# Kernel tuning notes

Hardware: AMD Instinct MI355X
Metric: run time of the kernel (lower is better)

Reference implementation:

```python
import jax, jax.numpy as jnp
import numpy as np

G, N, E = 64, 1000, 8192          # graphs, nodes/graph, edges/graph
F_IN, C, H, HID, NCLS = 128, 128, 4, 256, 2
EPS = 1e-5


def _gcn(x, src, dst, W, b):
    # GCNConv: symmetric normalization with self-loops, sum aggregation.
    h = x @ W                                              # [N, C]
    deg = jax.ops.segment_sum(jnp.ones(E, h.dtype), dst, num_segments=N) + 1.0
    dinv = jax.lax.rsqrt(deg)                              # deg^{-1/2}
    msg = h[src] * (dinv[src] * dinv[dst])[:, None]        # [E, C] gather
    out = jax.ops.segment_sum(msg, dst, num_segments=N)    # scatter-add
    out = out + h * (dinv * dinv)[:, None]                 # self-loop term
    return out + b


def _layernorm(y, g, b):
    mu = y.mean(-1, keepdims=True)
    var = ((y - mu) ** 2).mean(-1, keepdims=True)
    return (y - mu) * jax.lax.rsqrt(var + EPS) * g + b


def setup_inputs() -> dict:
    key = jax.random.key(0)
    ks = jax.random.split(key, 12)
    rn = lambda k, s: jax.random.normal(k, s, jnp.float32) * 0.05
    return dict(
        x=jax.random.normal(ks[0], (G, N, F_IN), jnp.float32),
        edge_index=jax.random.randint(ks[1], (G, 2, E), 0, N),
        W0=rn(ks[2], (F_IN, C)), b0=jnp.zeros((C,), jnp.float32),
        W1=rn(ks[3], (C, C)), b1=jnp.zeros((C,), jnp.float32),
        in_w=rn(ks[4], (3 * C, C)), in_b=jnp.zeros((3 * C,), jnp.float32),
        out_w=rn(ks[5], (C, C)), out_b=jnp.zeros((C,), jnp.float32),
        ln2_g=jnp.ones((C,), jnp.float32), ln2_b=jnp.zeros((C,), jnp.float32),
        mw1=rn(ks[6], (C, HID)), mb1=jnp.zeros((HID,), jnp.float32),
        mw2=rn(ks[7], (HID, C)), mb2=jnp.zeros((C,), jnp.float32),
        lw=rn(ks[8], (C, NCLS)), lb=jnp.zeros((NCLS,), jnp.float32),
    )


def reference(x, edge_index, W0, b0, W1, b1, in_w, in_b, out_w, out_b,
              ln2_g, ln2_b, mw1, mb1, mw2, mb2, lw, lb):
    src, dst = edge_index[:, 0, :], edge_index[:, 1, :]
    conv = jax.vmap(_gcn, in_axes=(0, 0, 0, None, None))
    h = jnp.tanh(conv(x, src, dst, W0, b0))   # [G, N, C]
    h = jnp.tanh(conv(h, src, dst, W1, b1))
    g = h.sum(axis=1)                          # SumAggregation -> [G, C]

    # MultiheadAttention, unbatched: sequence of G graph embeddings
    qkv = g @ in_w.T + in_b
    q, k, v = jnp.split(qkv, 3, axis=-1)
    d = C // H
    qh, kh, vh = (t.reshape(G, H, d) for t in (q, k, v))
    attn = jax.nn.softmax(jnp.einsum('qhd,khd->hqk', qh, kh) * (d ** -0.5), axis=-1)
    o = jnp.einsum('hqk,khd->qhd', attn, vh).reshape(G, C) @ out_w.T + out_b

    x_attend = o                               # dropout = identity (eval)
    # NOTE: original computes layer_norm1(x_attend) but immediately overwrites it.
    mlp = jnp.maximum(x_attend @ mw1 + mb1, 0.0) @ mw2 + mb2
    y = _layernorm(x_attend + mlp, ln2_g, ln2_b)
    node_repr = jnp.maximum(y, 0.0).sum(axis=0)  # [C]
    return node_repr @ lw + lb                   # [NCLS]
```

## Files before the change

kernel.cpp:

```cpp
#include <hip/hip_runtime.h>
#include <math.h>

#define Gn 64
#define Nn 1000
#define En 8192
#define Cc 128
#define HIDn 256
#define EPSf 1e-5f

typedef __attribute__((ext_vector_type(8))) short bh8;
typedef __attribute__((ext_vector_type(4))) float fx4;

__device__ __forceinline__ unsigned short f2bf(float f) {
    unsigned u = __float_as_uint(f);
    u += 0x7fffu + ((u >> 16) & 1u);
    return (unsigned short)(u >> 16);
}
__device__ __forceinline__ float bflo(unsigned u) { return __uint_as_float(u << 16); }
__device__ __forceinline__ float bfhi(unsigned u) { return __uint_as_float(u & 0xffff0000u); }
__device__ __forceinline__ float tanh_fast(float x) {
    float e = exp2f(x * 2.885390081777927f);
    return 1.f - 2.f * __builtin_amdgcn_rcpf(e + 1.f);
}

__global__ __launch_bounds__(256) void k_wt(const float* __restrict__ W0, const float* __restrict__ W1,
                                            unsigned short* __restrict__ Wt0g,
                                            unsigned short* __restrict__ Wt1g)
{
    __shared__ __align__(16) short Wls[128][136];
    int t = threadIdx.x;
    const float* Wsrc = (blockIdx.x == 0) ? W0 : W1;
    unsigned short* Wdst = (blockIdx.x == 0) ? Wt0g : Wt1g;
    for (int idx = t; idx < 16384; idx += 256) {
        int kI = idx >> 7, n = idx & 127;
        Wls[n][kI] = (short)f2bf(Wsrc[idx]);
    }
    __syncthreads();
    for (int idx = t; idx < 2048; idx += 256) {
        int n = idx >> 4, kc = idx & 15;
        *(bh8*)(Wdst + (size_t)idx * 8) = *(const bh8*)&Wls[n][kc * 8];
    }
}

__global__ __launch_bounds__(512) void k_front(const int* __restrict__ ei, const float* __restrict__ X,
                                               const unsigned short* __restrict__ Wt0g,
                                               int4* __restrict__ ninfo, int2* __restrict__ epair,
                                               float* __restrict__ pooled, float* __restrict__ repr,
                                               int* __restrict__ bars,
                                               unsigned short* __restrict__ Hout)
{
    __shared__ __align__(16) short Wt[128][136];
    __shared__ int wsum[8];
    int t = threadIdx.x;
    int b = blockIdx.x;

    if (b < 64) {
        int* curs = (int*)&Wt[0][0];
        float* dinv_s = (float*)((char*)&Wt[0][0] + 4096);
        int g = b;
        const int* srcp = ei + (size_t)g * 2 * En;
        const int* dstp = srcp + En;
        int lane = t & 63, wv = t >> 6;

        curs[t * 2] = 0; curs[t * 2 + 1] = 0;
        __syncthreads();
        for (int e = t; e < En; e += 512) atomicAdd(&curs[dstp[e]], 1);
        __syncthreads();

        int base = t * 2;
        int d0 = curs[base], d1 = curs[base + 1];
        int s = d0 + d1;
        int v = s;
        #pragma unroll
        for (int off = 1; off <= 32; off <<= 1) {
            int u = __shfl_up(v, off);
            if (lane >= off) v += u;
        }
        if (lane == 63) wsum[wv] = v;
        __syncthreads();
        int woff = 0;
        #pragma unroll
        for (int w = 0; w < 8; ++w) if (w < wv) woff += wsum[w];
        int e0 = woff + v - s;
        int e1 = e0 + d0;
        float dv0 = rsqrtf((float)d0 + 1.f), dv1 = rsqrtf((float)d1 + 1.f);
        curs[base] = e0; curs[base + 1] = e1;
        dinv_s[base] = dv0; dinv_s[base + 1] = dv1;
        if (base < Nn)     ninfo[g * Nn + base]     = make_int4(e0, d0, __float_as_int(dv0 * dv0), 0);
        if (base + 1 < Nn) ninfo[g * Nn + base + 1] = make_int4(e1, d1, __float_as_int(dv1 * dv1), 0);
        __syncthreads();

        for (int e = t; e < En; e += 512) {
            int dd = dstp[e], ss = srcp[e];
            int p = atomicAdd(&curs[dd], 1);
            float w = dinv_s[ss] * dinv_s[dd];
            epair[(size_t)g * En + p] = make_int2(ss << 8, __float_as_int(w));
        }
        if (t < Cc) pooled[g * Cc + t] = 0.f;
        if (g == 0 && t < Cc) repr[t] = 0.f;
        if (g == 0 && t < 4) bars[t] = 0;
        return;
    }

    int bb = b - 64;
    int xcd = bb & 7, gg = (bb >> 3) & 7, rblk = bb >> 6;
    int g = xcd + 8 * gg;
    for (int idx = t; idx < 2048; idx += 512) {
        int n = idx >> 4, kc = idx & 15;
        *(bh8*)&Wt[n][kc * 8] = *(const bh8*)(Wt0g + (size_t)idx * 8);
    }
    __syncthreads();

    int wave = t >> 6, l = t & 63;
    int lr = l & 15, lg = l >> 4;
    const float* Xf = X + (size_t)g * Nn * Cc;
    unsigned short* Hg = Hout + (size_t)g * Nn * Cc;

    int rbase = rblk * 128 + wave * 16;
    int r = rbase + lr;
    bool ok = r < Nn;
    bh8 af[4];
    #pragma unroll
    for (int ks = 0; ks < 4; ++ks) {
        if (ok) {
            const float* xp = Xf + (size_t)r * Cc + ks * 32 + lg * 8;
            fx4 a0 = *(const fx4*)xp;
            fx4 a1 = *(const fx4*)(xp + 4);
            bh8 av;
            av[0] = (short)f2bf(a0[0]); av[1] = (short)f2bf(a0[1]);
            av[2] = (short)f2bf(a0[2]); av[3] = (short)f2bf(a0[3]);
            av[4] = (short)f2bf(a1[0]); av[5] = (short)f2bf(a1[1]);
            av[6] = (short)f2bf(a1[2]); av[7] = (short)f2bf(a1[3]);
            af[ks] = av;
        } else af[ks] = bh8{0, 0, 0, 0, 0, 0, 0, 0};
    }
    fx4 acc[8];
    #pragma unroll
    for (int ct = 0; ct < 8; ++ct) acc[ct] = fx4{0.f, 0.f, 0.f, 0.f};
    #pragma unroll
    for (int ks = 0; ks < 4; ++ks) {
        #pragma unroll
        for (int ct = 0; ct < 8; ++ct) {
            bh8 bfr = *(const bh8*)(&Wt[ct * 16 + lr][ks * 32 + lg * 8]);
            acc[ct] = __builtin_amdgcn_mfma_f32_16x16x32_bf16(af[ks], bfr, acc[ct], 0, 0, 0);
        }
    }
    #pragma unroll
    for (int ct = 0; ct < 8; ++ct) {
        #pragma unroll
        for (int rg = 0; rg < 4; ++rg) {
            int row = rbase + lg * 4 + rg;
            if (row < Nn) Hg[(size_t)row * Cc + ct * 16 + lr] = f2bf(acc[ct][rg]);
        }
    }
}

__global__ __launch_bounds__(256) void k_gemm1(const unsigned short* __restrict__ Xh,
                                               const unsigned short* __restrict__ Wtg,
                                               unsigned short* __restrict__ Hout)
{
    __shared__ __align__(16) short Wt[128][136];
    int b = blockIdx.x;
    int xcd = b & 7, gg = (b >> 3) & 7, rblk = b >> 6;
    int g = xcd + 8 * gg;
    int t = threadIdx.x;
    for (int idx = t; idx < 2048; idx += 256) {
        int n = idx >> 4, kc = idx & 15;
        bh8 v = *(const bh8*)(Wtg + (size_t)idx * 8);
        *(bh8*)&Wt[n][kc * 8] = v;
    }
    __syncthreads();

    int wave = t >> 6, l = t & 63;
    int lr = l & 15, lg = l >> 4;
    const short* Xg = (const short*)Xh + (size_t)g * Nn * Cc;
    unsigned short* Hg = Hout + (size_t)g * Nn * Cc;

    int rbase = rblk * 64 + wave * 16;
    int r = rbase + lr;
    bool ok = r < Nn;
    bh8 af[4];
    #pragma unroll
    for (int ks = 0; ks < 4; ++ks) {
        if (ok) af[ks] = *(const bh8*)(Xg + (size_t)r * Cc + ks * 32 + lg * 8);
        else    af[ks] = bh8{0, 0, 0, 0, 0, 0, 0, 0};
    }
    fx4 acc[8];
    #pragma unroll
    for (int ct = 0; ct < 8; ++ct) acc[ct] = fx4{0.f, 0.f, 0.f, 0.f};
    #pragma unroll
    for (int ks = 0; ks < 4; ++ks) {
        #pragma unroll
        for (int ct = 0; ct < 8; ++ct) {
            bh8 bfr = *(const bh8*)(&Wt[ct * 16 + lr][ks * 32 + lg * 8]);
            acc[ct] = __builtin_amdgcn_mfma_f32_16x16x32_bf16(af[ks], bfr, acc[ct], 0, 0, 0);
        }
    }
    #pragma unroll
    for (int ct = 0; ct < 8; ++ct) {
        #pragma unroll
        for (int rg = 0; rg < 4; ++rg) {
            int row = rbase + lg * 4 + rg;
            if (row < Nn) Hg[(size_t)row * Cc + ct * 16 + lr] = f2bf(acc[ct][rg]);
        }
    }
}

template<int POOL>
__global__ __launch_bounds__(256) void k_combine(const unsigned* __restrict__ Hb, const int2* __restrict__ epair,
                                                 const int4* __restrict__ ninfo, const float* __restrict__ bias,
                                                 unsigned* __restrict__ Tout, float* __restrict__ pooled)
{
    int b = blockIdx.x;
    int xcd = b & 7, j = b >> 3;
    int g = xcd + 8 * (j & 7);
    int blk = j >> 3;
    int wave = threadIdx.x >> 6, lane = threadIdx.x & 63;
    const char* Hgc = (const char*)(Hb + (size_t)g * Nn * 64);
    const int2* epg = epair + (size_t)g * En;
    const int4* nig = ninfo + (size_t)g * Nn;
    float2 bb = *(const float2*)(bias + lane * 2);
    int lb4 = lane * 4;
    float px = 0.f, py = 0.f;
    for (int n = blk * 4 + wave; n < Nn; n += 128) {
        int4 ni = nig[n];
        int st = ni.x, dc = ni.y;
        float sw = __int_as_float(ni.z);
        unsigned hv = *(const unsigned*)(Hgc + n * 256 + lb4);
        float a0x = bflo(hv) * sw + bb.x, a0y = bfhi(hv) * sw + bb.y;
        float a1x = 0.f, a1y = 0.f, a2x = 0.f, a2y = 0.f, a3x = 0.f, a3y = 0.f;
        int e = 0;
        for (; e + 4 <= dc; e += 4) {
            int2 p0 = epg[st + e];
            int2 p1 = epg[st + e + 1];
            int2 p2 = epg[st + e + 2];
            int2 p3 = epg[st + e + 3];
            unsigned r0 = *(const unsigned*)(Hgc + p0.x + lb4);
            unsigned r1 = *(const unsigned*)(Hgc + p1.x + lb4);
            unsigned r2 = *(const unsigned*)(Hgc + p2.x + lb4);
            unsigned r3 = *(const unsigned*)(Hgc + p3.x + lb4);
            float w0 = __int_as_float(p0.y), w1 = __int_as_float(p1.y);
            float w2 = __int_as_float(p2.y), w3 = __int_as_float(p3.y);
            a0x = fmaf(bflo(r0), w0, a0x); a0y = fmaf(bfhi(r0), w0, a0y);
            a1x = fmaf(bflo(r1), w1, a1x); a1y = fmaf(bfhi(r1), w1, a1y);
            a2x = fmaf(bflo(r2), w2, a2x); a2y = fmaf(bfhi(r2), w2, a2y);
            a3x = fmaf(bflo(r3), w3, a3x); a3y = fmaf(bfhi(r3), w3, a3y);
        }
        for (; e < dc; ++e) {
            int2 p0 = epg[st + e];
            unsigned r0 = *(const unsigned*)(Hgc + p0.x + lb4);
            float w0 = __int_as_float(p0.y);
            a0x = fmaf(bflo(r0), w0, a0x); a0y = fmaf(bfhi(r0), w0, a0y);
        }
        float ax = (a0x + a1x) + (a2x + a3x);
        float ay = (a0y + a1y) + (a2y + a3y);
        float tx = tanh_fast(ax), ty = tanh_fast(ay);
        if (POOL) { px += tx; py += ty; }
        else Tout[(size_t)(g * Nn + n) * 64 + lane] = ((unsigned)f2bf(ty) << 16) | (unsigned)f2bf(tx);
    }
    if (POOL) {
        atomicAdd(&pooled[g * Cc + lane * 2], px);
        atomicAdd(&pooled[g * Cc + lane * 2 + 1], py);
    }
}

__global__ __launch_bounds__(1024) void k_qkv(const float* __restrict__ pooled, const float* __restrict__ in_w,
                                              const float* __restrict__ in_b, float* __restrict__ qkvb)
{
    int t = threadIdx.x, lane = t & 63, wv = t >> 6;
    int c = blockIdx.x * 16 + wv;
    const float* wr = in_w + c * Cc;
    float w0 = wr[lane], w1 = wr[64 + lane];
    float bias = in_b[c];
    for (int i = 0; i < Gn; ++i) {
        float p = fmaf(pooled[i * Cc + lane], w0, pooled[i * Cc + 64 + lane] * w1);
        #pragma unroll
        for (int off2 = 32; off2 > 0; off2 >>= 1) p += __shfl_xor(p, off2);
        if (lane == 0) qkvb[i * 384 + c] = p + bias;
    }
}

__global__ __launch_bounds__(512) void k_tail(const float* __restrict__ qkvb, const float* __restrict__ out_w,
                                              const float* __restrict__ out_b, const float* __restrict__ mw1,
                                              const float* __restrict__ mb1, const float* __restrict__ mw2,
                                              const float* __restrict__ mb2, const float* __restrict__ ln2g,
                                              const float* __restrict__ ln2b, const float* __restrict__ lw,
                                              const float* __restrict__ lb, float* __restrict__ repr,
                                              int* __restrict__ ctr, float* __restrict__ out)
{
    __shared__ float kk[64][129];
    __shared__ float vv[64][129];
    __shared__ float qrow[128];
    __shared__ float S[4][64];
    __shared__ float sob[128];
    __shared__ float sxatt[128];
    __shared__ float sm1p[2][256];
    __shared__ float sm1[256];
    __shared__ float sp2[4][128];
    __shared__ float yb[128];
    __shared__ int slast;
    int g = blockIdx.x;
    int t = threadIdx.x, lane = t & 63, wv = t >> 6;

    for (int idx = t; idx < 8192; idx += 512) {
        int i = idx >> 7, c = idx & 127;
        kk[i][c] = qkvb[i * 384 + 128 + c];
        vv[i][c] = qkvb[i * 384 + 256 + c];
    }
    if (t < 128) qrow[t] = qkvb[g * 384 + t];
    __syncthreads();

    if (t < 256) {
        int h = t >> 6, jj = t & 63;
        int base = h * 32;
        float acc = 0.f;
        #pragma unroll
        for (int d = 0; d < 32; ++d) acc = fmaf(qrow[base + d], kk[jj][base + d], acc);
        S[h][jj] = acc * 0.17677669529663687f;
    }
    __syncthreads();
    if (wv < 4) {
        float val = S[wv][lane];
        float m = val;
        #pragma unroll
        for (int off = 32; off > 0; off >>= 1) m = fmaxf(m, __shfl_xor(m, off));
        float e2 = expf(val - m);
        float ssum = e2;
        #pragma unroll
        for (int off = 32; off > 0; off >>= 1) ssum += __shfl_xor(ssum, off);
        S[wv][lane] = e2 / ssum;
    }
    __syncthreads();
    if (t < 128) {
        int h = t >> 5, d = t & 31;
        int col = h * 32 + d;
        float acc = 0.f;
        #pragma unroll 4
        for (int j = 0; j < 64; ++j) acc = fmaf(S[h][j], vv[j][col], acc);
        sob[col] = acc;
    }
    __syncthreads();

    {
        float o0 = sob[lane], o1 = sob[64 + lane];
        for (int c = wv; c < Cc; c += 8) {
            const float* wr = out_w + c * Cc;
            float p = fmaf(o0, wr[lane], o1 * wr[64 + lane]);
            #pragma unroll
            for (int off = 32; off > 0; off >>= 1) p += __shfl_xor(p, off);
            if (lane == 0) sxatt[c] = p + out_b[c];
        }
    }
    __syncthreads();

    {
        int jc = t & 255, half = t >> 8;
        int k0b = half * 64;
        float a[8];
        #pragma unroll
        for (int u = 0; u < 8; ++u) a[u] = 0.f;
        for (int k0 = k0b; k0 < k0b + 64; k0 += 8) {
            #pragma unroll
            for (int u = 0; u < 8; ++u)
                a[u] = fmaf(sxatt[k0 + u], mw1[(size_t)(k0 + u) * HIDn + jc], a[u]);
        }
        sm1p[half][jc] = ((a[0] + a[1]) + (a[2] + a[3])) + ((a[4] + a[5]) + (a[6] + a[7]));
        __syncthreads();
        if (t < 256) sm1[t] = fmaxf(sm1p[0][t] + sm1p[1][t] + mb1[t], 0.f);
    }
    __syncthreads();

    {
        int c = t & 127, q = t >> 7;
        int j0b = q * 64;
        float a[8];
        #pragma unroll
        for (int u = 0; u < 8; ++u) a[u] = 0.f;
        for (int j0 = j0b; j0 < j0b + 64; j0 += 8) {
            #pragma unroll
            for (int u = 0; u < 8; ++u)
                a[u] = fmaf(sm1[j0 + u], mw2[(size_t)(j0 + u) * Cc + c], a[u]);
        }
        sp2[q][c] = ((a[0] + a[1]) + (a[2] + a[3])) + ((a[4] + a[5]) + (a[6] + a[7]));
        __syncthreads();
        if (t < 128) yb[t] = sxatt[t] + (sp2[0][t] + sp2[1][t]) + (sp2[2][t] + sp2[3][t]) + mb2[t];
    }
    __syncthreads();

    if (t < 64) {
        float v0 = yb[lane], v1 = yb[64 + lane];
        float s = v0 + v1;
        #pragma unroll
        for (int off = 32; off > 0; off >>= 1) s += __shfl_xor(s, off);
        float mu = s * (1.f / 128.f);
        float d0 = v0 - mu, d1 = v1 - mu;
        float vvr = d0 * d0 + d1 * d1;
        #pragma unroll
        for (int off = 32; off > 0; off >>= 1) vvr += __shfl_xor(vvr, off);
        float rstd = rsqrtf(vvr * (1.f / 128.f) + EPSf);
        float z0 = fmaxf(d0 * rstd * ln2g[lane] + ln2b[lane], 0.f);
        float z1 = fmaxf(d1 * rstd * ln2g[64 + lane] + ln2b[64 + lane], 0.f);
        atomicAdd(&repr[lane], z0);
        atomicAdd(&repr[64 + lane], z1);
    }

    __threadfence();
    __syncthreads();
    if (t == 0) slast = atomicAdd(ctr, 1);
    __syncthreads();
    if (slast == 63) {
        __threadfence();
        __shared__ float r0s[128], r1s[128];
        if (t < 128) {
            float r = __hip_atomic_load(&repr[t], __ATOMIC_RELAXED, __HIP_MEMORY_SCOPE_AGENT);
            r0s[t] = r * lw[t * 2 + 0];
            r1s[t] = r * lw[t * 2 + 1];
        }
        __syncthreads();
        for (int s2 = 64; s2 > 0; s2 >>= 1) {
            if (t < s2) { r0s[t] += r0s[t + s2]; r1s[t] += r1s[t + s2]; }
            __syncthreads();
        }
        if (t == 0) { out[0] = r0s[0] + lb[0]; out[1] = r1s[0] + lb[1]; }
    }
}

extern "C" void kernel_launch(void* const* d_in, const int* in_sizes, int n_in,
                              void* d_out, int out_size, void* d_ws, size_t ws_size,
                              hipStream_t stream)
{
    const float* x     = (const float*)d_in[0];
    const int*   ei    = (const int*)d_in[1];
    const float* W0    = (const float*)d_in[2];
    const float* b0    = (const float*)d_in[3];
    const float* W1    = (const float*)d_in[4];
    const float* b1    = (const float*)d_in[5];
    const float* in_w  = (const float*)d_in[6];
    const float* in_b  = (const float*)d_in[7];
    const float* out_w = (const float*)d_in[8];
    const float* out_b = (const float*)d_in[9];
    const float* ln2g  = (const float*)d_in[10];
    const float* ln2b  = (const float*)d_in[11];
    const float* mw1   = (const float*)d_in[12];
    const float* mb1   = (const float*)d_in[13];
    const float* mw2   = (const float*)d_in[14];
    const float* mb2   = (const float*)d_in[15];
    const float* lw    = (const float*)d_in[16];
    const float* lb    = (const float*)d_in[17];
    float* out = (float*)d_out;
    (void)in_sizes; (void)n_in; (void)out_size; (void)ws_size;

    char* ws = (char*)d_ws;
    size_t off = 0;
    auto carve = [&](size_t bytes) { size_t o = off; off += (bytes + 255) & ~(size_t)255; return o; };
    size_t o_ni    = carve((size_t)Gn * Nn * 16);
    size_t o_ep    = carve((size_t)Gn * En * 8);
    size_t o_pool  = carve((size_t)Gn * Cc * 4);
    size_t o_qkv   = carve((size_t)Gn * 384 * 4);
    size_t o_repr  = carve((size_t)Cc * 4);
    size_t o_bars  = carve(256);
    size_t o_W0t   = carve((size_t)Cc * Cc * 2);
    size_t o_W1t   = carve((size_t)Cc * Cc * 2);
    size_t o_H     = carve((size_t)Gn * Nn * Cc * 2);
    size_t o_T     = carve((size_t)Gn * Nn * Cc * 2);

    int4*  ninfo  = (int4*)(ws + o_ni);
    int2*  epair  = (int2*)(ws + o_ep);
    float* pooled = (float*)(ws + o_pool);
    float* qkvb   = (float*)(ws + o_qkv);
    float* repr   = (float*)(ws + o_repr);
    int*   bars   = (int*)(ws + o_bars);
    unsigned short* Wt0g = (unsigned short*)(ws + o_W0t);
    unsigned short* Wt1g = (unsigned short*)(ws + o_W1t);
    unsigned short* H  = (unsigned short*)(ws + o_H);
    unsigned short* T  = (unsigned short*)(ws + o_T);

    k_wt<<<2, 256, 0, stream>>>(W0, W1, Wt0g, Wt1g);
    k_front<<<576, 512, 0, stream>>>(ei, x, Wt0g, ninfo, epair, pooled, repr, bars, H);
    k_combine<0><<<2048, 256, 0, stream>>>((const unsigned*)H, epair, ninfo, b0, (unsigned*)T, nullptr);
    k_gemm1<<<1024, 256, 0, stream>>>(T, Wt1g, H);
    k_combine<1><<<2048, 256, 0, stream>>>((const unsigned*)H, epair, ninfo, b1, nullptr, pooled);
    k_qkv<<<24, 1024, 0, stream>>>(pooled, in_w, in_b, qkvb);
    k_tail<<<64, 512, 0, stream>>>(qkvb, out_w, out_b, mw1, mb1, mw2, mb2, ln2g, ln2b,
                                   lw, lb, repr, &bars[2], out);
}
```

Before: 152.0 us.

## Fuse first-layer aggregation with second GEMM via shared-memory tile

Merges the layer-0 edge aggregation and tanh with the layer-1 GEMM into one kernel. Each block aggregates 64 node rows into an LDS bf16 tile, then runs MFMA against the W1 tile and writes H2 directly. This drops the global write and re-read of the intermediate T buffer and one kernel launch. In exchange each block does the irregular gather work serially per wave (8 rows per wave) before the GEMM, so the gather phase has less parallelism and latency hiding than the separate 2048-block combine kernel had.

```diff
diff --git a/kernel.cpp b/kernel.cpp
--- a/kernel.cpp
+++ b/kernel.cpp
@@ -155,61 +155,109 @@
     }
 }
 
-__global__ __launch_bounds__(256) void k_gemm1(const unsigned short* __restrict__ Xh,
-                                               const unsigned short* __restrict__ Wtg,
-                                               unsigned short* __restrict__ Hout)
+__global__ __launch_bounds__(512) void k_cg1(const unsigned* __restrict__ Hb, const int2* __restrict__ epair,
+                                             const int4* __restrict__ ninfo, const float* __restrict__ bias,
+                                             const unsigned short* __restrict__ Wtg,
+                                             unsigned short* __restrict__ Hout)
 {
     __shared__ __align__(16) short Wt[128][136];
+    __shared__ __align__(16) short Tl[64][136];
     int b = blockIdx.x;
     int xcd = b & 7, gg = (b >> 3) & 7, rblk = b >> 6;
     int g = xcd + 8 * gg;
-    int t = threadIdx.x;
-    for (int idx = t; idx < 2048; idx += 256) {
+    int t = threadIdx.x, wv = t >> 6, lane = t & 63;
+
+    for (int idx = t; idx < 2048; idx += 512) {
         int n = idx >> 4, kc = idx & 15;
-        bh8 v = *(const bh8*)(Wtg + (size_t)idx * 8);
-        *(bh8*)&Wt[n][kc * 8] = v;
-    }
-    __syncthreads();
-
-    int wave = t >> 6, l = t & 63;
-    int lr = l & 15, lg = l >> 4;
-    const short* Xg = (const short*)Xh + (size_t)g * Nn * Cc;
-    unsigned short* Hg = Hout + (size_t)g * Nn * Cc;
-
-    int rbase = rblk * 64 + wave * 16;
-    int r = rbase + lr;
-    bool ok = r < Nn;
-    bh8 af[4];
-    #pragma unroll
-    for (int ks = 0; ks < 4; ++ks) {
-        if (ok) af[ks] = *(const bh8*)(Xg + (size_t)r * Cc + ks * 32 + lg * 8);
-        else    af[ks] = bh8{0, 0, 0, 0, 0, 0, 0, 0};
-    }
-    fx4 acc[8];
-    #pragma unroll
-    for (int ct = 0; ct < 8; ++ct) acc[ct] = fx4{0.f, 0.f, 0.f, 0.f};
-    #pragma unroll
-    for (int ks = 0; ks < 4; ++ks) {
-        #pragma unroll
-        for (int ct = 0; ct < 8; ++ct) {
-            bh8 bfr = *(const bh8*)(&Wt[ct * 16 + lr][ks * 32 + lg * 8]);
-            acc[ct] = __builtin_amdgcn_mfma_f32_16x16x32_bf16(af[ks], bfr, acc[ct], 0, 0, 0);
-        }
-    }
-    #pragma unroll
-    for (int ct = 0; ct < 8; ++ct) {
-        #pragma unroll
-        for (int rg = 0; rg < 4; ++rg) {
-            int row = rbase + lg * 4 + rg;
-            if (row < Nn) Hg[(size_t)row * Cc + ct * 16 + lr] = f2bf(acc[ct][rg]);
-        }
-    }
-}
-
-template<int POOL>
-__global__ __launch_bounds__(256) void k_combine(const unsigned* __restrict__ Hb, const int2* __restrict__ epair,
-                                                 const int4* __restrict__ ninfo, const float* __restrict__ bias,
-                                                 unsigned* __restrict__ Tout, float* __restrict__ pooled)
+        *(bh8*)&Wt[n][kc * 8] = *(const bh8*)(Wtg + (size_t)idx * 8);
+    }
+    __syncthreads();
+
+    {
+        const char* Hgc = (const char*)(Hb + (size_t)g * Nn * 64);
+        const int2* epg = epair + (size_t)g * En;
+        const int4* nig = ninfo + (size_t)g * Nn;
+        float2 bb = *(const float2*)(bias + lane * 2);
+        int lb4 = lane * 4;
+        int rbase = rblk * 64;
+        for (int i = 0; i < 8; ++i) {
+            int lrow = wv * 8 + i;
+            int n = rbase + lrow;
+            unsigned packed = 0;
+            if (n < Nn) {
+                int4 ni = nig[n];
+                int st = ni.x, dc = ni.y;
+                float sw = __int_as_float(ni.z);
+                unsigned hv = *(const unsigned*)(Hgc + n * 256 + lb4);
+                float a0x = bflo(hv) * sw + bb.x, a0y = bfhi(hv) * sw + bb.y;
+                float a1x = 0.f, a1y = 0.f, a2x = 0.f, a2y = 0.f, a3x = 0.f, a3y = 0.f;
+                int e = 0;
+                for (; e + 4 <= dc; e += 4) {
+                    int2 p0 = epg[st + e];
+                    int2 p1 = epg[st + e + 1];
+                    int2 p2 = epg[st + e + 2];
+                    int2 p3 = epg[st + e + 3];
+                    unsigned r0 = *(const unsigned*)(Hgc + p0.x + lb4);
+                    unsigned r1 = *(const unsigned*)(Hgc + p1.x + lb4);
+                    unsigned r2 = *(const unsigned*)(Hgc + p2.x + lb4);
+                    unsigned r3 = *(const unsigned*)(Hgc + p3.x + lb4);
+                    float w0 = __int_as_float(p0.y), w1 = __int_as_float(p1.y);
+                    float w2 = __int_as_float(p2.y), w3 = __int_as_float(p3.y);
+                    a0x = fmaf(bflo(r0), w0, a0x); a0y = fmaf(bfhi(r0), w0, a0y);
+                    a1x = fmaf(bflo(r1), w1, a1x); a1y = fmaf(bfhi(r1), w1, a1y);
+                    a2x = fmaf(bflo(r2), w2, a2x); a2y = fmaf(bfhi(r2), w2, a2y);
+                    a3x = fmaf(bflo(r3), w3, a3x); a3y = fmaf(bfhi(r3), w3, a3y);
+                }
+                for (; e < dc; ++e) {
+                    int2 p0 = epg[st + e];
+                    unsigned r0 = *(const unsigned*)(Hgc + p0.x + lb4);
+                    float w0 = __int_as_float(p0.y);
+                    a0x = fmaf(bflo(r0), w0, a0x); a0y = fmaf(bfhi(r0), w0, a0y);
+                }
+                float ax = (a0x + a1x) + (a2x + a3x);
+                float ay = (a0y + a1y) + (a2y + a3y);
+                packed = ((unsigned)f2bf(tanh_fast(ay)) << 16) | (unsigned)f2bf(tanh_fast(ax));
+            }
+            *(unsigned*)&Tl[lrow][lane * 2] = packed;
+        }
+    }
+    __syncthreads();
+
+    {
+        int lr = lane & 15, lg = lane >> 4;
+        int tb = (wv & 3) * 16;
+        int ctb = (wv >> 2) * 4;
+        unsigned short* Hg = Hout + (size_t)g * Nn * Cc;
+        int rbase = rblk * 64;
+
+        bh8 af[4];
+        #pragma unroll
+        for (int ks = 0; ks < 4; ++ks) af[ks] = *(const bh8*)&Tl[tb + lr][ks * 32 + lg * 8];
+        fx4 acc[4];
+        #pragma unroll
+        for (int c2 = 0; c2 < 4; ++c2) acc[c2] = fx4{0.f, 0.f, 0.f, 0.f};
+        #pragma unroll
+        for (int ks = 0; ks < 4; ++ks) {
+            #pragma unroll
+            for (int c2 = 0; c2 < 4; ++c2) {
+                bh8 bfr = *(const bh8*)(&Wt[(ctb + c2) * 16 + lr][ks * 32 + lg * 8]);
+                acc[c2] = __builtin_amdgcn_mfma_f32_16x16x32_bf16(af[ks], bfr, acc[c2], 0, 0, 0);
+            }
+        }
+        #pragma unroll
+        for (int c2 = 0; c2 < 4; ++c2) {
+            #pragma unroll
+            for (int rg = 0; rg < 4; ++rg) {
+                int row = rbase + tb + lg * 4 + rg;
+                if (row < Nn) Hg[(size_t)row * Cc + (ctb + c2) * 16 + lr] = f2bf(acc[c2][rg]);
+            }
+        }
+    }
+}
+
+__global__ __launch_bounds__(256) void k_combine1(const unsigned* __restrict__ Hb, const int2* __restrict__ epair,
+                                                  const int4* __restrict__ ninfo, const float* __restrict__ bias,
+                                                  float* __restrict__ pooled)
 {
     int b = blockIdx.x;
     int xcd = b & 7, j = b >> 3;
@@ -254,14 +302,11 @@
         }
         float ax = (a0x + a1x) + (a2x + a3x);
         float ay = (a0y + a1y) + (a2y + a3y);
-        float tx = tanh_fast(ax), ty = tanh_fast(ay);
-        if (POOL) { px += tx; py += ty; }
-        else Tout[(size_t)(g * Nn + n) * 64 + lane] = ((unsigned)f2bf(ty) << 16) | (unsigned)f2bf(tx);
-    }
-    if (POOL) {
-        atomicAdd(&pooled[g * Cc + lane * 2], px);
-        atomicAdd(&pooled[g * Cc + lane * 2 + 1], py);
-    }
+        px += tanh_fast(ax);
+        py += tanh_fast(ay);
+    }
+    atomicAdd(&pooled[g * Cc + lane * 2], px);
+    atomicAdd(&pooled[g * Cc + lane * 2 + 1], py);
 }
 
 __global__ __launch_bounds__(1024) void k_qkv(const float* __restrict__ pooled, const float* __restrict__ in_w,
@@ -462,7 +507,7 @@
     size_t o_W0t   = carve((size_t)Cc * Cc * 2);
     size_t o_W1t   = carve((size_t)Cc * Cc * 2);
     size_t o_H     = carve((size_t)Gn * Nn * Cc * 2);
-    size_t o_T     = carve((size_t)Gn * Nn * Cc * 2);
+    size_t o_H2    = carve((size_t)Gn * Nn * Cc * 2);
 
     int4*  ninfo  = (int4*)(ws + o_ni);
     int2*  epair  = (int2*)(ws + o_ep);
@@ -473,13 +518,12 @@
     unsigned short* Wt0g = (unsigned short*)(ws + o_W0t);
     unsigned short* Wt1g = (unsigned short*)(ws + o_W1t);
     unsigned short* H  = (unsigned short*)(ws + o_H);
-    unsigned short* T  = (unsigned short*)(ws + o_T);
+    unsigned short* H2 = (unsigned short*)(ws + o_H2);
 
     k_wt<<<2, 256, 0, stream>>>(W0, W1, Wt0g, Wt1g);
     k_front<<<576, 512, 0, stream>>>(ei, x, Wt0g, ninfo, epair, pooled, repr, bars, H);
-    k_combine<0><<<2048, 256, 0, stream>>>((const unsigned*)H, epair, ninfo, b0, (unsigned*)T, nullptr);
-    k_gemm1<<<1024, 256, 0, stream>>>(T, Wt1g, H);
-    k_combine<1><<<2048, 256, 0, stream>>>((const unsigned*)H, epair, ninfo, b1, nullptr, pooled);
+    k_cg1<<<1024, 512, 0, stream>>>((const unsigned*)H, epair, ninfo, b0, Wt1g, H2);
+    k_combine1<<<2048, 256, 0, stream>>>((const unsigned*)H2, epair, ninfo, b1, pooled);
     k_qkv<<<24, 1024, 0, stream>>>(pooled, in_w, in_b, qkvb);
     k_tail<<<64, 512, 0, stream>>>(qkvb, out_w, out_b, mw1, mb1, mw2, mb2, ln2g, ln2b,
                                    lw, lb, repr, &bars[2], out);
```

After: 162.0 us. +6.6%, slower.
